# Performance work log

Hardware: AMD Instinct MI355X
Metric: run time of the kernel (lower is better)

Reference implementation:

```python
import jax, jax.numpy as jnp
import numpy as np

D_MODEL = 1024
N_HEADS = 16
HEAD_DIM = D_MODEL // N_HEADS
D_FF = 4 * D_MODEL
LN_EPS = 1e-5


def _linear_params(key, d_in, d_out):
    kw, kb = jax.random.split(key)
    bound = 1.0 / np.sqrt(d_in)
    W = jax.random.uniform(kw, (d_out, d_in), jnp.float32, -bound, bound)
    b = jax.random.uniform(kb, (d_out,), jnp.float32, -bound, bound)
    return W, b


def setup_inputs() -> dict:
    key = jax.random.key(0)
    ks = jax.random.split(key, 8)
    x = jax.random.normal(ks[0], (4, 2048, D_MODEL), jnp.float32)
    Wq, bq = _linear_params(ks[1], D_MODEL, D_MODEL)
    Wk, bk = _linear_params(ks[2], D_MODEL, D_MODEL)
    Wv, bv = _linear_params(ks[3], D_MODEL, D_MODEL)
    Wo, bo = _linear_params(ks[4], D_MODEL, D_MODEL)
    W1, b1 = _linear_params(ks[5], D_MODEL, D_FF)
    W2, b2 = _linear_params(ks[6], D_FF, D_MODEL)
    ln1_g = jnp.ones((D_MODEL,), jnp.float32)
    ln1_b = jnp.zeros((D_MODEL,), jnp.float32)
    ln2_g = jnp.ones((D_MODEL,), jnp.float32)
    ln2_b = jnp.zeros((D_MODEL,), jnp.float32)
    return dict(x=x, Wq=Wq, bq=bq, Wk=Wk, bk=bk, Wv=Wv, bv=bv, Wo=Wo, bo=bo,
                W1=W1, b1=b1, W2=W2, b2=b2,
                ln1_g=ln1_g, ln1_b=ln1_b, ln2_g=ln2_g, ln2_b=ln2_b)


def _layernorm(x, g, b):
    mu = jnp.mean(x, axis=-1, keepdims=True)
    var = jnp.mean(jnp.square(x - mu), axis=-1, keepdims=True)
    return (x - mu) * jax.lax.rsqrt(var + LN_EPS) * g + b


def reference(x, Wq, bq, Wk, bk, Wv, bv, Wo, bo, W1, b1, W2, b2,
              ln1_g, ln1_b, ln2_g, ln2_b):
    B, S, D = x.shape
    # project and split heads -> [B, H, S, hd]
    def heads(W, b):
        return (jnp.einsum('bsd,ed->bse', x, W) + b).reshape(B, S, N_HEADS, HEAD_DIM).transpose(0, 2, 1, 3)
    Q, K, V = heads(Wq, bq), heads(Wk, bk), heads(Wv, bv)
    scores = jnp.einsum('bhqd,bhkd->bhqk', Q, K) / np.sqrt(HEAD_DIM).astype(np.float32)
    causal = jnp.tril(jnp.ones((S, S), jnp.bool_))  # True where attending allowed
    scores = jnp.where(causal, scores, -jnp.inf)
    weights = jax.nn.softmax(scores, axis=-1)  # dropout = identity in eval mode
    attn = jnp.einsum('bhqk,bhkd->bhqd', weights, V)
    attn = attn.transpose(0, 2, 1, 3).reshape(B, S, D)
    att_out = jnp.einsum('bsd,ed->bse', attn, Wo) + bo
    x1 = _layernorm(x + att_out, ln1_g, ln1_b)
    h = jax.nn.gelu(jnp.einsum('bsd,fd->bsf', x1, W1) + b1, approximate=False)
    ff_out = jnp.einsum('bsf,df->bsd', h, W2) + b2
    x2 = _layernorm(ff_out + x1, ln2_g, ln2_b)
    return x2  # final dropout = identity in eval mode
```

## Files before the change

kernel.cpp:

```cpp
#include <hip/hip_runtime.h>
#include <hip/hip_bf16.h>


typedef unsigned short u16;
typedef unsigned int u32;
typedef short s16x8 __attribute__((ext_vector_type(8)));
typedef float f32x4 __attribute__((ext_vector_type(4)));
typedef float f32x16 __attribute__((ext_vector_type(16)));
typedef unsigned short u16x8 __attribute__((ext_vector_type(8)));
typedef unsigned short u16x4 __attribute__((ext_vector_type(4)));
typedef unsigned int u32x4 __attribute__((ext_vector_type(4)));

#define MFMA16(a, b, c) __builtin_amdgcn_mfma_f32_16x16x32_bf16(a, b, c, 0, 0, 0)
#define MFMA32(a, b, c) __builtin_amdgcn_mfma_f32_32x32x16_bf16(a, b, c, 0, 0, 0)

#define GLDS16(g, l)                                                     \
  __builtin_amdgcn_global_load_lds(                                     \
      (const __attribute__((address_space(1))) unsigned int*)(g),       \
      (__attribute__((address_space(3))) unsigned int*)(l), 16, 0, 0)

__device__ __forceinline__ u16 f2bf(float f) {
  unsigned u = __builtin_bit_cast(unsigned, f);
  u += 0x7fffu + ((u >> 16) & 1u);
  return (u16)(u >> 16);
}

__device__ __forceinline__ int swz(int b) { return b ^ (((b >> 7) & 7) << 4); }

struct CvtArgs {
  const float* src[7];
  u16* dst[7];
  int start[8];
};

__global__ __launch_bounds__(256) void cvt_all(CvtArgs a) {
  int b = blockIdx.x;
  int r = 0;
#pragma unroll
  for (int i = 1; i < 7; i++) r += (b >= a.start[i]);
  long i = (long)(b - a.start[r]) * 256 + threadIdx.x;
  const float4* s = (const float4*)a.src[r];
  float4 va = s[2 * i], vb = s[2 * i + 1];
  u16x8 o;
  o[0] = f2bf(va.x); o[1] = f2bf(va.y); o[2] = f2bf(va.z); o[3] = f2bf(va.w);
  o[4] = f2bf(vb.x); o[5] = f2bf(vb.y); o[6] = f2bf(vb.z); o[7] = f2bf(vb.w);
  ((u16x8*)a.dst[r])[i] = o;
}

template <int EPI>
__global__ __launch_bounds__(256) void gemm_bt(
    const u16* __restrict__ A, const u16* __restrict__ Bt, int K,
    const float* __restrict__ c0, const float* __restrict__ c1,
    const float* __restrict__ c2, const float* __restrict__ resid,
    u16* __restrict__ ob0, u16* __restrict__ ob1, u16* __restrict__ ob2,
    float* __restrict__ of) {
  __shared__ u16 As[128 * 32];
  __shared__ u16 Bs[128 * 32];
  const int tid = threadIdx.x, w = tid >> 6, l = tid & 63;
  const int wr = w >> 1, wc = w & 1;
  const long row0 = (long)blockIdx.x * 128, col0 = (long)blockIdx.y * 128;

  f32x4 acc[4][4];
#pragma unroll
  for (int i = 0; i < 4; i++)
#pragma unroll
    for (int j = 0; j < 4; j++) acc[i][j] = f32x4{0.f, 0.f, 0.f, 0.f};

  const u16* Ag = A + (row0 + w * 32 + (l >> 2)) * (long)K + (l & 3) * 8;
  const u16* Bg = Bt + (col0 + w * 32 + (l >> 2)) * (long)K + (l & 3) * 8;
  char* AsB = (char*)As + w * 2048;
  char* BsB = (char*)Bs + w * 2048;

  for (int k0 = 0; k0 < K; k0 += 32) {
    GLDS16(Ag + k0, AsB);
    GLDS16(Ag + k0 + 16 * (long)K, AsB + 1024);
    GLDS16(Bg + k0, BsB);
    GLDS16(Bg + k0 + 16 * (long)K, BsB + 1024);
    __syncthreads();
    s16x8 af[4], bfr[4];
#pragma unroll
    for (int mi = 0; mi < 4; mi++)
      af[mi] = *(const s16x8*)((const char*)As +
                               ((wr * 64 + mi * 16 + (l & 15)) * 64 + ((l >> 4) * 16)));
#pragma unroll
    for (int ni = 0; ni < 4; ni++)
      bfr[ni] = *(const s16x8*)((const char*)Bs +
                                ((wc * 64 + ni * 16 + (l & 15)) * 64 + ((l >> 4) * 16)));
#pragma unroll
    for (int mi = 0; mi < 4; mi++)
#pragma unroll
      for (int ni = 0; ni < 4; ni++)
        acc[mi][ni] = MFMA16(af[mi], bfr[ni], acc[mi][ni]);
    __syncthreads();
  }

#pragma unroll
  for (int mi = 0; mi < 4; mi++)
#pragma unroll
    for (int ni = 0; ni < 4; ni++) {
      long rbase = row0 + wr * 64 + mi * 16 + ((l >> 4) << 2);
      long col = col0 + wc * 64 + ni * 16 + (l & 15);
#pragma unroll
      for (int r = 0; r < 4; r++) {
        long row = rbase + r;
        float v = acc[mi][ni][r];
        if constexpr (EPI == 0) {
          int which = (int)(col >> 10);
          int ec = (int)(col & 1023);
          const float* bias = which == 0 ? c0 : (which == 1 ? c1 : c2);
          v += bias[ec];
          if (which == 0) v *= 0.125f;
          int hh = ec >> 6, dd = ec & 63;
          long bb = row >> 11, sl = row & 2047;
          if (which == 2) {
            ob2[(((bb * 16 + hh) * 64 + dd) << 11) + sl] = f2bf(v);
          } else {
            u16* dst = which == 0 ? ob0 : ob1;
            dst[(((bb * 16 + hh) * 2048 + sl) << 6) + dd] = f2bf(v);
          }
        } else if constexpr (EPI == 1) {
          v += c0[col] + resid[row * 1024 + col];
          of[row * 1024 + col] = v;
        } else if constexpr (EPI == 2) {
          v += c0[col];
          v = 0.5f * v * (1.f + erff(v * 0.70710678118654752f));
          ob0[row * 4096 + col] = f2bf(v);
        } else {
          v += c0[col] + resid[row * 1024 + col];
          of[row * 1024 + col] = v;
        }
      }
    }
}

__global__ __launch_bounds__(256, 4) void attn2_kernel(const u16* __restrict__ Qb,
                                                       const u16* __restrict__ Kb,
                                                       const u16* __restrict__ Vbt,
                                                       u16* __restrict__ attb) {
  __shared__ u16 Kt[2][64 * 64];
  __shared__ u16 Vt[2][64 * 64];

  const int tid = threadIdx.x, w = tid >> 6, l = tid & 63;
  const int hi = l >> 5, ln = l & 31;
  const int bh = blockIdx.y;
  const int qt = (int)gridDim.x - 1 - (int)blockIdx.x;
  const int q0w = qt * 128 + w * 32;
  const int q = q0w + ln;
  const long kbase = (long)bh * (2048 * 64);
  const long vbase = (long)bh * (64 * 2048);
  const int tmax = 2 * qt + 1;
  const int cs = (l & 7) ^ ((l >> 3) & 7);

  s16x8 qf[4];
  {
    const char* qp = (const char*)(Qb + kbase) + (long)q * 128 + hi * 16;
#pragma unroll
    for (int kk = 0; kk < 4; kk++) qf[kk] = *(const s16x8*)(qp + kk * 32);
  }

  f32x16 acc0, acc1;
#pragma unroll
  for (int i = 0; i < 16; i++) { acc0[i] = 0.f; acc1[i] = 0.f; }
  float mrow = -1e30f, lsum = 0.f;

  const u16* kg = Kb + kbase;
  const u16* vg = Vbt + vbase;
#define STAGE(bf, t)                                                            \
  {                                                                             \
    int s0_ = (t) * 64;                                                         \
    GLDS16(kg + (long)(s0_ + w * 16 + (l >> 3)) * 64 + cs * 8,                  \
           (char*)Kt[bf] + w * 2048);                                           \
    GLDS16(kg + (long)(s0_ + w * 16 + 8 + (l >> 3)) * 64 + cs * 8,              \
           (char*)Kt[bf] + w * 2048 + 1024);                                    \
    GLDS16(vg + (long)(w * 16 + (l >> 3)) * 2048 + s0_ + cs * 8,                \
           (char*)Vt[bf] + w * 2048);                                           \
    GLDS16(vg + (long)(w * 16 + 8 + (l >> 3)) * 2048 + s0_ + cs * 8,            \
           (char*)Vt[bf] + w * 2048 + 1024);                                    \
  }

  STAGE(0, 0);

  for (int t = 0; t <= tmax; ++t) {
    __syncthreads();
    const int cur = t & 1;
    if (t < tmax) STAGE(cur ^ 1, t + 1);
    if (64 * t > q0w + 31) continue;
    const int s0 = t * 64;

    f32x16 p0, p1;
#pragma unroll
    for (int i = 0; i < 16; i++) { p0[i] = 0.f; p1[i] = 0.f; }
#pragma unroll
    for (int kk = 0; kk < 4; kk++) {
      s16x8 kf0 = *(const s16x8*)((char*)Kt[cur] + swz(ln * 128 + kk * 32 + hi * 16));
      s16x8 kf1 = *(const s16x8*)((char*)Kt[cur] + swz((32 + ln) * 128 + kk * 32 + hi * 16));
      p0 = MFMA32(kf0, qf[kk], p0);
      p1 = MFMA32(kf1, qf[kk], p1);
    }

    if (s0 + 63 > q0w) {
#pragma unroll
      for (int r = 0; r < 16; r++) {
        int so = (r & 3) + 8 * (r >> 2) + 4 * hi;
        if (s0 + so > q) p0[r] = -1e30f;
        if (s0 + 32 + so > q) p1[r] = -1e30f;
      }
    }

    float mt = -1e30f;
#pragma unroll
    for (int r = 0; r < 16; r++) { mt = fmaxf(mt, p0[r]); mt = fmaxf(mt, p1[r]); }
    mt = fmaxf(mt, __shfl_xor(mt, 32, 64));
    float mnew = fmaxf(mrow, mt);
    float corr = __expf(mrow - mnew);
    float lp = 0.f;
#pragma unroll
    for (int r = 0; r < 16; r++) {
      p0[r] = __expf(p0[r] - mnew); lp += p0[r];
      p1[r] = __expf(p1[r] - mnew); lp += p1[r];
    }
    lp += __shfl_xor(lp, 32, 64);
    lsum = lsum * corr + lp;
    mrow = mnew;
#pragma unroll
    for (int i = 0; i < 16; i++) { acc0[i] *= corr; acc1[i] *= corr; }

    u32x4 pa[4];
#pragma unroll
    for (int kb = 0; kb < 4; kb++) {
      const int b8 = 8 * (kb & 1);
#pragma unroll
      for (int tt = 0; tt < 2; tt++) {
        float a0, a1, b0, b1;
        if (kb < 2) {
          a0 = p0[b8 + 2 * tt]; a1 = p0[b8 + 2 * tt + 1];
          b0 = p0[b8 + 4 + 2 * tt]; b1 = p0[b8 + 5 + 2 * tt];
        } else {
          a0 = p1[b8 + 2 * tt]; a1 = p1[b8 + 2 * tt + 1];
          b0 = p1[b8 + 4 + 2 * tt]; b1 = p1[b8 + 5 + 2 * tt];
        }
        u32 X = (u32)f2bf(a0) | ((u32)f2bf(a1) << 16);
        u32 Y = (u32)f2bf(b0) | ((u32)f2bf(b1) << 16);
        u32 Xx = __shfl_xor(X, 32, 64), Yx = __shfl_xor(Y, 32, 64);
        pa[kb][tt]     = (hi == 0) ? X : Yx;
        pa[kb][tt + 2] = (hi == 0) ? Xx : Y;
      }
    }

#pragma unroll
    for (int kb = 0; kb < 4; kb++) {
      s16x8 pf = __builtin_bit_cast(s16x8, pa[kb]);
      s16x8 vf0 = *(const s16x8*)((char*)Vt[cur] + swz(ln * 128 + kb * 32 + hi * 16));
      s16x8 vf1 = *(const s16x8*)((char*)Vt[cur] + swz((32 + ln) * 128 + kb * 32 + hi * 16));
      acc0 = MFMA32(vf0, pf, acc0);
      acc1 = MFMA32(vf1, pf, acc1);
    }
  }

  const float inv = 1.0f / lsum;
  const long orow = ((long)(bh >> 4) * 2048 + q) * 1024 + (bh & 15) * 64;
#pragma unroll
  for (int dblk = 0; dblk < 2; dblk++) {
#pragma unroll
    for (int rq = 0; rq < 4; rq++) {
      u16x4 o;
#pragma unroll
      for (int e = 0; e < 4; e++) {
        float v = (dblk == 0 ? acc0[rq * 4 + e] : acc1[rq * 4 + e]) * inv;
        o[e] = f2bf(v);
      }
      int d = 32 * dblk + 8 * rq + 4 * hi;
      *(u16x4*)(attb + orow + d) = o;
    }
  }
#undef STAGE
}

__global__ __launch_bounds__(256) void ln_kernel(const float* __restrict__ in,
                                                 float* __restrict__ outf,
                                                 u16* __restrict__ outb,
                                                 const float* __restrict__ g,
                                                 const float* __restrict__ be) {
  __shared__ float a1[4], a2[4];
  long row = blockIdx.x;
  const float4* p = (const float4*)(in + row * 1024);
  int t = threadIdx.x, w = t >> 6, l = t & 63;
  float4 v = p[t];
  float s = v.x + v.y + v.z + v.w;
#pragma unroll
  for (int off = 1; off < 64; off <<= 1) s += __shfl_xor(s, off, 64);
  if (l == 0) a1[w] = s;
  __syncthreads();
  float mu = (a1[0] + a1[1] + a1[2] + a1[3]) * (1.f / 1024.f);
  float d0 = v.x - mu, d1 = v.y - mu, d2 = v.z - mu, d3 = v.w - mu;
  float q = d0 * d0 + d1 * d1 + d2 * d2 + d3 * d3;
#pragma unroll
  for (int off = 1; off < 64; off <<= 1) q += __shfl_xor(q, off, 64);
  if (l == 0) a2[w] = q;
  __syncthreads();
  float var = (a2[0] + a2[1] + a2[2] + a2[3]) * (1.f / 1024.f);
  float rs = rsqrtf(var + 1e-5f);
  float4 gg = ((const float4*)g)[t], bb = ((const float4*)be)[t];
  float o0 = d0 * rs * gg.x + bb.x, o1 = d1 * rs * gg.y + bb.y;
  float o2 = d2 * rs * gg.z + bb.z, o3 = d3 * rs * gg.w + bb.w;
  if (outf) {
    float4 o; o.x = o0; o.y = o1; o.z = o2; o.w = o3;
    ((float4*)(outf + row * 1024))[t] = o;
  }
  if (outb) {
    u16x4 u; u[0] = f2bf(o0); u[1] = f2bf(o1); u[2] = f2bf(o2); u[3] = f2bf(o3);
    ((u16x4*)outb)[row * 256 + t] = u;
  }
}

extern "C" void kernel_launch(void* const* d_in, const int* in_sizes, int n_in,
                              void* d_out, int out_size, void* d_ws, size_t ws_size,
                              hipStream_t stream) {
  const float* x   = (const float*)d_in[0];
  const float* Wq  = (const float*)d_in[1];
  const float* bq  = (const float*)d_in[2];
  const float* Wk  = (const float*)d_in[3];
  const float* bk  = (const float*)d_in[4];
  const float* Wv  = (const float*)d_in[5];
  const float* bv  = (const float*)d_in[6];
  const float* Wo  = (const float*)d_in[7];
  const float* bo  = (const float*)d_in[8];
  const float* W1  = (const float*)d_in[9];
  const float* b1  = (const float*)d_in[10];
  const float* W2  = (const float*)d_in[11];
  const float* b2  = (const float*)d_in[12];
  const float* g1  = (const float*)d_in[13];
  const float* be1 = (const float*)d_in[14];
  const float* g2  = (const float*)d_in[15];
  const float* be2 = (const float*)d_in[16];

  char* ws = (char*)d_ws;
  const size_t MB = 1ull << 20;
  u16*   wb_qkv = (u16*)(ws + 0);
  u16*   wb_o   = (u16*)(ws + 6 * MB);
  u16*   wb_1   = (u16*)(ws + 8 * MB);
  u16*   wb_2   = (u16*)(ws + 16 * MB);
  u16*   xb     = (u16*)(ws + 24 * MB);
  u16*   attb   = (u16*)(ws + 40 * MB);
  float* x1f    = (float*)(ws + 56 * MB);
  u16*   qb     = (u16*)(ws + 88 * MB);
  u16*   kb     = (u16*)(ws + 104 * MB);
  u16*   vbt    = (u16*)(ws + 120 * MB);
  u16*   hb     = (u16*)(ws + 88 * MB);
  float* outf   = (float*)d_out;

  CvtArgs ca;
  ca.src[0] = Wq; ca.dst[0] = wb_qkv;
  ca.src[1] = Wk; ca.dst[1] = wb_qkv + 1048576;
  ca.src[2] = Wv; ca.dst[2] = wb_qkv + 2097152;
  ca.src[3] = Wo; ca.dst[3] = wb_o;
  ca.src[4] = W1; ca.dst[4] = wb_1;
  ca.src[5] = W2; ca.dst[5] = wb_2;
  ca.src[6] = x;  ca.dst[6] = xb;
  ca.start[0] = 0;    ca.start[1] = 512;  ca.start[2] = 1024; ca.start[3] = 1536;
  ca.start[4] = 2048; ca.start[5] = 4096; ca.start[6] = 6144; ca.start[7] = 10240;
  cvt_all<<<10240, 256, 0, stream>>>(ca);

  gemm_bt<0><<<dim3(64, 24), 256, 0, stream>>>(xb, wb_qkv, 1024, bq, bk, bv,
                                               nullptr, qb, kb, vbt, nullptr);
  attn2_kernel<<<dim3(16, 64), 256, 0, stream>>>(qb, kb, vbt, attb);
  gemm_bt<1><<<dim3(64, 8), 256, 0, stream>>>(attb, wb_o, 1024, bo, nullptr, nullptr,
                                              x, nullptr, nullptr, nullptr, x1f);
  ln_kernel<<<8192, 256, 0, stream>>>(x1f, x1f, xb, g1, be1);
  gemm_bt<2><<<dim3(64, 32), 256, 0, stream>>>(xb, wb_1, 1024, b1, nullptr, nullptr,
                                               nullptr, hb, nullptr, nullptr, nullptr);
  gemm_bt<3><<<dim3(64, 8), 256, 0, stream>>>(hb, wb_2, 4096, b2, nullptr, nullptr,
                                              x1f, nullptr, nullptr, nullptr, outf);
  ln_kernel<<<8192, 256, 0, stream>>>(outf, outf, nullptr, g2, be2);
}
```

Baseline: 607.7 us.

## Rewrite GEMM with double-buffered K=64 tiles, 8 waves, and XCD-aware block remap

Replaces the 128x128x32 single-buffered GEMM with a 512-thread version that double-buffers 128x64 A/B tiles in LDS, prefetching the next K tile while computing the current one. It also remaps the linear block index so consecutive tiles on each XCD share rows, to improve L2 reuse. Each wave now computes a 32x64 sub-tile, which means more waves and fewer accumulators per wave. The cost is 64KB of LDS per block, which may limit occupancy, and the LDS reads stay unswizzled, so bank conflicts may remain.

```diff
diff --git a/kernel.cpp b/kernel.cpp
--- a/kernel.cpp
+++ b/kernel.cpp
@@ -48,58 +48,69 @@
 }
 
 template <int EPI>
-__global__ __launch_bounds__(256) void gemm_bt(
-    const u16* __restrict__ A, const u16* __restrict__ Bt, int K,
+__global__ __launch_bounds__(512, 4) void gemm2(
+    const u16* __restrict__ A, const u16* __restrict__ Bt, int K, int NB,
     const float* __restrict__ c0, const float* __restrict__ c1,
     const float* __restrict__ c2, const float* __restrict__ resid,
     u16* __restrict__ ob0, u16* __restrict__ ob1, u16* __restrict__ ob2,
     float* __restrict__ of) {
-  __shared__ u16 As[128 * 32];
-  __shared__ u16 Bs[128 * 32];
+  __shared__ u16 As[2][128 * 64];
+  __shared__ u16 Bs[2][128 * 64];
   const int tid = threadIdx.x, w = tid >> 6, l = tid & 63;
-  const int wr = w >> 1, wc = w & 1;
-  const long row0 = (long)blockIdx.x * 128, col0 = (long)blockIdx.y * 128;
-
-  f32x4 acc[4][4];
-#pragma unroll
-  for (int i = 0; i < 4; i++)
+  const int wrow = w >> 1, wcol = w & 1;
+  const int nwg = gridDim.x, cpx = nwg >> 3, lid = blockIdx.x;
+  const int sid = (lid & 7) * cpx + (lid >> 3);
+  const long row0 = (long)(sid / NB) * 128, col0 = (long)(sid % NB) * 128;
+
+  f32x4 acc[2][4];
+#pragma unroll
+  for (int i = 0; i < 2; i++)
 #pragma unroll
     for (int j = 0; j < 4; j++) acc[i][j] = f32x4{0.f, 0.f, 0.f, 0.f};
 
-  const u16* Ag = A + (row0 + w * 32 + (l >> 2)) * (long)K + (l & 3) * 8;
-  const u16* Bg = Bt + (col0 + w * 32 + (l >> 2)) * (long)K + (l & 3) * 8;
-  char* AsB = (char*)As + w * 2048;
-  char* BsB = (char*)Bs + w * 2048;
-
-  for (int k0 = 0; k0 < K; k0 += 32) {
-    GLDS16(Ag + k0, AsB);
-    GLDS16(Ag + k0 + 16 * (long)K, AsB + 1024);
-    GLDS16(Bg + k0, BsB);
-    GLDS16(Bg + k0 + 16 * (long)K, BsB + 1024);
+  const u16* Ag = A + (row0 + w * 8 + (l >> 3)) * (long)K + (l & 7) * 8;
+  const u16* Bg = Bt + (col0 + w * 8 + (l >> 3)) * (long)K + (l & 7) * 8;
+
+#define STAGE2(bf, k0)                                                \
+  GLDS16(Ag + (k0),                &As[bf][(w * 8) * 64]);            \
+  GLDS16(Ag + (k0) + 64 * (long)K, &As[bf][(64 + w * 8) * 64]);       \
+  GLDS16(Bg + (k0),                &Bs[bf][(w * 8) * 64]);            \
+  GLDS16(Bg + (k0) + 64 * (long)K, &Bs[bf][(64 + w * 8) * 64]);
+
+  const int nt = K >> 6;
+  int cur = 0;
+  STAGE2(0, 0)
+  __syncthreads();
+  for (int t = 0; t < nt; ++t) {
+    if (t + 1 < nt) { STAGE2(cur ^ 1, (t + 1) << 6) }
+#pragma unroll
+    for (int ks = 0; ks < 2; ks++) {
+      s16x8 af[2], bfr[4];
+#pragma unroll
+      for (int mi = 0; mi < 2; mi++)
+        af[mi] = *(const s16x8*)(&As[cur][(wrow * 32 + mi * 16 + (l & 15)) * 64 +
+                                          ks * 32 + (l >> 4) * 8]);
+#pragma unroll
+      for (int ni = 0; ni < 4; ni++)
+        bfr[ni] = *(const s16x8*)(&Bs[cur][(wcol * 64 + ni * 16 + (l & 15)) * 64 +
+                                           ks * 32 + (l >> 4) * 8]);
+#pragma unroll
+      for (int mi = 0; mi < 2; mi++)
+#pragma unroll
+        for (int ni = 0; ni < 4; ni++)
+          acc[mi][ni] = MFMA16(af[mi], bfr[ni], acc[mi][ni]);
+    }
     __syncthreads();
-    s16x8 af[4], bfr[4];
-#pragma unroll
-    for (int mi = 0; mi < 4; mi++)
-      af[mi] = *(const s16x8*)((const char*)As +
-                               ((wr * 64 + mi * 16 + (l & 15)) * 64 + ((l >> 4) * 16)));
-#pragma unroll
-    for (int ni = 0; ni < 4; ni++)
-      bfr[ni] = *(const s16x8*)((const char*)Bs +
-                                ((wc * 64 + ni * 16 + (l & 15)) * 64 + ((l >> 4) * 16)));
-#pragma unroll
-    for (int mi = 0; mi < 4; mi++)
-#pragma unroll
-      for (int ni = 0; ni < 4; ni++)
-        acc[mi][ni] = MFMA16(af[mi], bfr[ni], acc[mi][ni]);
-    __syncthreads();
-  }
-
-#pragma unroll
-  for (int mi = 0; mi < 4; mi++)
+    cur ^= 1;
+  }
+#undef STAGE2
+
+#pragma unroll
+  for (int mi = 0; mi < 2; mi++)
 #pragma unroll
     for (int ni = 0; ni < 4; ni++) {
-      long rbase = row0 + wr * 64 + mi * 16 + ((l >> 4) << 2);
-      long col = col0 + wc * 64 + ni * 16 + (l & 15);
+      long rbase = row0 + wrow * 32 + mi * 16 + ((l >> 4) << 2);
+      long col = col0 + wcol * 64 + ni * 16 + (l & 15);
 #pragma unroll
       for (int r = 0; r < 4; r++) {
         long row = rbase + r;
@@ -361,15 +372,15 @@
   ca.start[4] = 2048; ca.start[5] = 4096; ca.start[6] = 6144; ca.start[7] = 10240;
   cvt_all<<<10240, 256, 0, stream>>>(ca);
 
-  gemm_bt<0><<<dim3(64, 24), 256, 0, stream>>>(xb, wb_qkv, 1024, bq, bk, bv,
-                                               nullptr, qb, kb, vbt, nullptr);
+  gemm2<0><<<1536, 512, 0, stream>>>(xb, wb_qkv, 1024, 24, bq, bk, bv,
+                                     nullptr, qb, kb, vbt, nullptr);
   attn2_kernel<<<dim3(16, 64), 256, 0, stream>>>(qb, kb, vbt, attb);
-  gemm_bt<1><<<dim3(64, 8), 256, 0, stream>>>(attb, wb_o, 1024, bo, nullptr, nullptr,
-                                              x, nullptr, nullptr, nullptr, x1f);
+  gemm2<1><<<512, 512, 0, stream>>>(attb, wb_o, 1024, 8, bo, nullptr, nullptr,
+                                    x, nullptr, nullptr, nullptr, x1f);
   ln_kernel<<<8192, 256, 0, stream>>>(x1f, x1f, xb, g1, be1);
-  gemm_bt<2><<<dim3(64, 32), 256, 0, stream>>>(xb, wb_1, 1024, b1, nullptr, nullptr,
-                                               nullptr, hb, nullptr, nullptr, nullptr);
-  gemm_bt<3><<<dim3(64, 8), 256, 0, stream>>>(hb, wb_2, 4096, b2, nullptr, nullptr,
-                                              x1f, nullptr, nullptr, nullptr, outf);
+  gemm2<2><<<2048, 512, 0, stream>>>(xb, wb_1, 1024, 32, b1, nullptr, nullptr,
+                                     nullptr, hb, nullptr, nullptr, nullptr);
+  gemm2<3><<<512, 512, 0, stream>>>(hb, wb_2, 4096, 8, b2, nullptr, nullptr,
+                                    x1f, nullptr, nullptr, nullptr, outf);
   ln_kernel<<<8192, 256, 0, stream>>>(outf, outf, nullptr, g2, be2);
 }
```

New measurement: 670.1 us. 1.1x slower.
